# Kernel tuning notes

Hardware: AMD Instinct MI355X
Metric: run time of the kernel (lower is better)

The kernel has to match this reference:

```python
import math
import jax, jax.numpy as jnp
import numpy as np

NUM_HEADS = 32
HIDDEN = 4096
HEAD_DIM = HIDDEN // NUM_HEADS  # 128
NEG_INF = -1e30


def _alibi_slopes(n: int) -> jnp.ndarray:
    cp2 = 2 ** math.floor(math.log2(n))
    base = 2.0 ** (-(2.0 ** (-(math.log2(cp2) - 3))))
    slopes = base ** np.arange(1, cp2 + 1, dtype=np.float64)
    if cp2 != n:
        extra_base = 2.0 ** (-(2.0 ** (-(math.log2(2 * cp2) - 3))))
        rem = min(cp2, n - cp2)
        extra = extra_base ** np.arange(1, 1 + 2 * rem, 2, dtype=np.float64)
        slopes = np.concatenate([slopes, extra])
    return jnp.asarray(slopes, dtype=jnp.float32)


def setup_inputs() -> dict:
    key = jax.random.key(0)
    k1, k2, k3 = jax.random.split(key, 3)
    B, S = 2, 2048
    hidden_states = jax.random.normal(k1, (B, S, HIDDEN), dtype=jnp.float32)
    Wqkv = jax.random.normal(k2, (HIDDEN, NUM_HEADS * HEAD_DIM + 2 * HEAD_DIM), dtype=jnp.float32) * 0.02
    Wo = jax.random.normal(k3, (HIDDEN, HIDDEN), dtype=jnp.float32) * 0.02
    return {"hidden_states": hidden_states, "Wqkv": Wqkv, "Wo": Wo}


def reference(hidden_states, Wqkv, Wo):
    B, S, H = hidden_states.shape
    nH, d = NUM_HEADS, HEAD_DIM
    scale = d ** -0.5

    qkv = hidden_states @ Wqkv                      # [B,S,nH*d + 2d]
    q = qkv[..., : nH * d].reshape(B, S, nH, d)     # [B,S,nH,d]
    k = qkv[..., nH * d: nH * d + d]                # [B,S,d] (single kv head, MQA)
    v = qkv[..., nH * d + d:]                       # [B,S,d]

    scores = jnp.einsum("bqhd,bkd->bhqk", q, k) * scale  # [B,nH,S,S]

    pos_q = jnp.arange(S)[:, None]
    pos_k = jnp.arange(S)[None, :]
    slopes = _alibi_slopes(nH)                       # [nH]
    alibi = slopes[:, None, None] * (pos_k - pos_q).astype(jnp.float32)  # [nH,S,S]
    causal = pos_k <= pos_q                          # [S,S]

    scores = jnp.where(causal[None, None], scores + alibi[None], NEG_INF)
    probs = jax.nn.softmax(scores, axis=-1)
    attn = jnp.einsum("bhqk,bkd->bqhd", probs, v).reshape(B, S, H)
    return attn @ Wo
```

## Files before the change

kernel.cpp:

```cpp
#include <hip/hip_runtime.h>
#include <hip/hip_bf16.h>

typedef __attribute__((ext_vector_type(8))) short bf16x8;
typedef __attribute__((ext_vector_type(4))) float f32x4;
typedef __attribute__((ext_vector_type(8))) unsigned short u16x8;
typedef __attribute__((ext_vector_type(4))) unsigned short u16x4;

__device__ __forceinline__ unsigned short f2bf(float x) {
    union { float f; unsigned u; } v; v.f = x;
    unsigned r = v.u + 0x7fff + ((v.u >> 16) & 1);
    return (unsigned short)(r >> 16);
}

__device__ __forceinline__ unsigned short f2bf_hw(float x) {
    __hip_bfloat16 h = __float2bfloat16(x);
    return *reinterpret_cast<unsigned short*>(&h);
}

__device__ __forceinline__ void gload16(const void* g, void* l) {
    __builtin_amdgcn_global_load_lds(
        (const __attribute__((address_space(1))) void*)g,
        (__attribute__((address_space(3))) void*)l, 16, 0, 0);
}

__global__ __launch_bounds__(256) void cast_bf16_kernel(
    const float* __restrict__ src, unsigned short* __restrict__ dst, int n8) {
    int i = blockIdx.x * 256 + threadIdx.x;
    if (i >= n8) return;
    const float4* s = (const float4*)src + (size_t)i * 2;
    float4 a = s[0], b = s[1];
    u16x8 o;
    o[0] = f2bf(a.x); o[1] = f2bf(a.y); o[2] = f2bf(a.z); o[3] = f2bf(a.w);
    o[4] = f2bf(b.x); o[5] = f2bf(b.y); o[6] = f2bf(b.z); o[7] = f2bf(b.w);
    *(u16x8*)(dst + (size_t)i * 8) = o;
}

__global__ __launch_bounds__(256) void transpose_cast_kernel(
    const float* __restrict__ src, unsigned short* __restrict__ dst, int R, int C) {
    __shared__ float tile[32][33];
    const int bx = blockIdx.x * 32, by = blockIdx.y * 32;
    const int tx = threadIdx.x & 31, ty = threadIdx.x >> 5;
#pragma unroll
    for (int i = 0; i < 32; i += 8)
        tile[ty + i][tx] = src[(size_t)(by + ty + i) * C + (bx + tx)];
    __syncthreads();
#pragma unroll
    for (int i = 0; i < 32; i += 8)
        dst[(size_t)(bx + ty + i) * R + (by + tx)] = f2bf(tile[tx][ty + i]);
}

template <int OUTBF>
__global__ __launch_bounds__(256) void gemm_kernel(
    const unsigned short* __restrict__ A, const unsigned short* __restrict__ BT,
    void* __restrict__ Cp, int M, int N, int K) {
    __shared__ unsigned short Al[2][128 * 32];
    __shared__ unsigned short Bl[2][128 * 32];
    const int t = threadIdx.x;
    const int wid = t >> 6, lane = t & 63;
    const int l15 = lane & 15, lg = lane >> 4;
    const int bm = blockIdx.y * 128, bn = blockIdx.x * 128;
    const int wm = (wid >> 1) * 64, wn = (wid & 1) * 64;

    f32x4 acc[4][4];
#pragma unroll
    for (int i = 0; i < 4; ++i)
#pragma unroll
        for (int j = 0; j < 4; ++j) acc[i][j] = (f32x4)(0.f);

    const int nk = K >> 5;
    const int c0 = t, c1 = t + 256;

    auto stage = [&](int buf, int kt) {
        const unsigned short* Ab = A + (size_t)bm * K + kt * 32;
        const unsigned short* Bb = BT + (size_t)bn * K + kt * 32;
        gload16(Ab + (size_t)(c0 >> 2) * K + (c0 & 3) * 8, &Al[buf][wid * 64 * 8]);
        gload16(Ab + (size_t)(c1 >> 2) * K + (c1 & 3) * 8, &Al[buf][(256 + wid * 64) * 8]);
        gload16(Bb + (size_t)(c0 >> 2) * K + (c0 & 3) * 8, &Bl[buf][wid * 64 * 8]);
        gload16(Bb + (size_t)(c1 >> 2) * K + (c1 & 3) * 8, &Bl[buf][(256 + wid * 64) * 8]);
    };

    stage(0, 0);
    __syncthreads();
    for (int kt = 0; kt < nk; ++kt) {
        const int cur = kt & 1;
        if (kt + 1 < nk) stage(cur ^ 1, kt + 1);
        bf16x8 af[4], bfr[4];
#pragma unroll
        for (int i = 0; i < 4; ++i) {
            af[i]  = *(const bf16x8*)&Al[cur][(wm + i * 16 + l15) * 32 + lg * 8];
            bfr[i] = *(const bf16x8*)&Bl[cur][(wn + i * 16 + l15) * 32 + lg * 8];
        }
#pragma unroll
        for (int i = 0; i < 4; ++i)
#pragma unroll
            for (int j = 0; j < 4; ++j)
                acc[i][j] = __builtin_amdgcn_mfma_f32_16x16x32_bf16(af[i], bfr[j], acc[i][j], 0, 0, 0);
        __syncthreads();
    }

#pragma unroll
    for (int i = 0; i < 4; ++i)
#pragma unroll
        for (int j = 0; j < 4; ++j)
#pragma unroll
            for (int r = 0; r < 4; ++r) {
                const int row = bm + wm + i * 16 + lg * 4 + r;
                const int col = bn + wn + j * 16 + l15;
                if (OUTBF) ((unsigned short*)Cp)[(size_t)row * N + col] = f2bf(acc[i][j][r]);
                else       ((float*)Cp)[(size_t)row * N + col] = acc[i][j][r];
            }
}

__global__ __launch_bounds__(256, 4) void attn_kernel(
    const unsigned short* __restrict__ qkv, unsigned short* __restrict__ attn, int S) {
    constexpr int LD = 4352;
    __shared__ unsigned short Kl[64 * 128];
    __shared__ unsigned short Vt[128 * 64];
    __shared__ unsigned short Pl[4][16 * 64];
    const int t = threadIdx.x, wid = t >> 6;
    const int lane = t & 63, l15 = lane & 15, lg = lane >> 4;
    const int h = blockIdx.y, b = blockIdx.z;
    const size_t rb = (size_t)b * S;
    const int nQB = S >> 6;
    const float scale2 = 0.08838834764831845f * 1.4426950408889634f;
    const float slope2 = exp2f(-0.25f * (float)(h + 1)) * 1.4426950408889634f;
    const float sr1 = slope2, sr2 = slope2 * 2.f, sr3 = slope2 * 3.f;

    for (int half = 0; half < 2; ++half) {
        const int qblk = half ? (nQB - 1 - (int)blockIdx.x) : (int)blockIdx.x;
        const int q0w = qblk * 64 + wid * 16;
        const int qlane = q0w + l15;
        const float aq = slope2 * (float)qlane;

        bf16x8 qf[4];
        {
            const unsigned short* qrow = qkv + (rb + qlane) * LD + h * 128 + lg * 8;
#pragma unroll
            for (int j = 0; j < 4; ++j) qf[j] = *(const bf16x8*)(qrow + j * 32);
        }
        f32x4 o[8];
#pragma unroll
        for (int i = 0; i < 8; ++i) o[i] = (f32x4)(0.f);
        float m_ = -1e30f, l_ = 0.f;

        const int ntile = qblk + 1;
        for (int tile = 0; tile < ntile; ++tile) {
            const int t0 = tile * 64;
            {
                const char* kbase = (const char*)(qkv + (rb + t0) * LD + 4096);
#pragma unroll
                for (int i = 0; i < 4; ++i) {
                    const int c = i * 256 + t;
                    const int krow = c >> 4;
                    gload16(kbase + (size_t)krow * (LD * 2) + (((c & 15) * 16) ^ ((krow & 7) << 4)),
                            (char*)Kl + (i * 256 + wid * 64) * 16);
                }
            }
            {
                const unsigned short* vs = qkv + (rb + t0 + lane) * LD + 4224 + wid * 32;
                u16x8 v0 = *(const u16x8*)vs;
                u16x8 v1 = *(const u16x8*)(vs + 8);
                u16x8 v2 = *(const u16x8*)(vs + 16);
                u16x8 v3 = *(const u16x8*)(vs + 24);
                const int kb = 2 * lane;
#pragma unroll
                for (int e = 0; e < 8; ++e) {
                    int dd = wid * 32 + e;
                    *(unsigned short*)((char*)Vt + dd * 128 + (kb ^ ((dd & 7) << 4))) = v0[e];
                    dd += 8;
                    *(unsigned short*)((char*)Vt + dd * 128 + (kb ^ ((dd & 7) << 4))) = v1[e];
                    dd += 8;
                    *(unsigned short*)((char*)Vt + dd * 128 + (kb ^ ((dd & 7) << 4))) = v2[e];
                    dd += 8;
                    *(unsigned short*)((char*)Vt + dd * 128 + (kb ^ ((dd & 7) << 4))) = v3[e];
                }
            }
            __syncthreads();

            f32x4 s4[4];
#pragma unroll
            for (int ct = 0; ct < 4; ++ct) {
                s4[ct] = (f32x4)(0.f);
                const int row = ct * 16 + l15;
                const int swz = (row & 7) << 4;
#pragma unroll
                for (int j = 0; j < 4; ++j) {
                    bf16x8 kf = *(const bf16x8*)((const char*)Kl + row * 256 +
                                                 ((j * 64 + lg * 16) ^ swz));
                    s4[ct] = __builtin_amdgcn_mfma_f32_16x16x32_bf16(kf, qf[j], s4[ct], 0, 0, 0);
                }
            }

            const float base = slope2 * (float)(t0 + lg * 4) - aq;
            float p4[4][4];
            float mx = -1e30f;
            const bool lastt = (tile == ntile - 1);
            const int dbase = t0 + lg * 4 - qlane;
#pragma unroll
            for (int ct = 0; ct < 4; ++ct) {
                const float bbc = base + slope2 * 16.f * (float)ct;
#pragma unroll
                for (int r = 0; r < 4; ++r) {
                    float sc = fmaf(s4[ct][r], scale2,
                                    bbc + (r == 0 ? 0.f : (r == 1 ? sr1 : (r == 2 ? sr2 : sr3))));
                    if (lastt && (dbase + ct * 16 + r > 0)) sc = -1e30f;
                    p4[ct][r] = sc;
                    mx = fmaxf(mx, sc);
                }
            }
            mx = fmaxf(mx, __shfl_xor(mx, 16));
            mx = fmaxf(mx, __shfl_xor(mx, 32));

            if (!__all(mx <= m_ + 8.0f)) {
                const float mnew = fmaxf(m_, mx);
                const float corr = exp2f(m_ - mnew);
                m_ = mnew;
                l_ *= corr;
                float cr[4];
#pragma unroll
                for (int r = 0; r < 4; ++r) cr[r] = __shfl(corr, lg * 4 + r);
#pragma unroll
                for (int n = 0; n < 8; ++n) {
                    o[n][0] *= cr[0]; o[n][1] *= cr[1];
                    o[n][2] *= cr[2]; o[n][3] *= cr[3];
                }
            }

            float rs = 0.f;
#pragma unroll
            for (int ct = 0; ct < 4; ++ct)
#pragma unroll
                for (int r = 0; r < 4; ++r) {
                    const float pv = exp2f(p4[ct][r] - m_);
                    p4[ct][r] = pv;
                    rs += pv;
                }
            rs += __shfl_xor(rs, 16);
            rs += __shfl_xor(rs, 32);
            l_ += rs;

            {
                char* pb = (char*)&Pl[wid][0] + l15 * 128;
                const int swz = (l15 & 7) << 4;
#pragma unroll
                for (int ct = 0; ct < 4; ++ct) {
                    u16x4 w;
                    w[0] = f2bf_hw(p4[ct][0]); w[1] = f2bf_hw(p4[ct][1]);
                    w[2] = f2bf_hw(p4[ct][2]); w[3] = f2bf_hw(p4[ct][3]);
                    *(u16x4*)(pb + ((ct * 32 + lg * 8) ^ swz)) = w;
                }
            }

            const char* pb = (const char*)&Pl[wid][0] + l15 * 128;
            const int pswz = (l15 & 7) << 4;
            bf16x8 pa0 = *(const bf16x8*)(pb + ((lg * 16) ^ pswz));
            bf16x8 pa1 = *(const bf16x8*)(pb + ((64 + lg * 16) ^ pswz));
#pragma unroll
            for (int n = 0; n < 8; ++n) {
                const int dd = n * 16 + l15;
                const int vswz = (dd & 7) << 4;
                bf16x8 vf0 = *(const bf16x8*)((const char*)Vt + dd * 128 + ((lg * 16) ^ vswz));
                bf16x8 vf1 = *(const bf16x8*)((const char*)Vt + dd * 128 + ((64 + lg * 16) ^ vswz));
                f32x4 a4 = __builtin_amdgcn_mfma_f32_16x16x32_bf16(pa0, vf0, o[n], 0, 0, 0);
                o[n] = __builtin_amdgcn_mfma_f32_16x16x32_bf16(pa1, vf1, a4, 0, 0, 0);
            }
            __syncthreads();
        }

        const float rl = 1.f / l_;
        float rv[4];
#pragma unroll
        for (int r = 0; r < 4; ++r) rv[r] = __shfl(rl, lg * 4 + r);
#pragma unroll
        for (int n = 0; n < 8; ++n)
#pragma unroll
            for (int r = 0; r < 4; ++r) {
                const int q = q0w + lg * 4 + r;
                attn[(rb + q) * 4096 + h * 128 + n * 16 + l15] = f2bf(o[n][r] * rv[r]);
            }
    }
}

extern "C" void kernel_launch(void* const* d_in, const int* in_sizes, int n_in,
                              void* d_out, int out_size, void* d_ws, size_t ws_size,
                              hipStream_t stream) {
    const float* hidden = (const float*)d_in[0];
    const float* Wqkv   = (const float*)d_in[1];
    const float* Wo     = (const float*)d_in[2];
    float* out = (float*)d_out;
    char* ws = (char*)d_ws;

    const int B = 2, S = 2048, H = 4096, NQ = 4352;
    const int M = B * S;

    unsigned short* hb  = (unsigned short*)(ws);
    unsigned short* wT  = (unsigned short*)(ws + 33554432);
    unsigned short* qkv = (unsigned short*)(ws + 33554432 + 35651584);

    cast_bf16_kernel<<<(M * H / 8) / 256, 256, 0, stream>>>(hidden, hb, M * H / 8);
    transpose_cast_kernel<<<dim3(NQ / 32, H / 32), 256, 0, stream>>>(Wqkv, wT, H, NQ);
    gemm_kernel<1><<<dim3(NQ / 128, M / 128), 256, 0, stream>>>(hb, wT, qkv, M, NQ, H);
    transpose_cast_kernel<<<dim3(H / 32, H / 32), 256, 0, stream>>>(Wo, wT, H, H);
    attn_kernel<<<dim3(16, 32, 2), 256, 0, stream>>>(qkv, hb, S);
    gemm_kernel<0><<<dim3(H / 128, M / 128), 256, 0, stream>>>(hb, wT, out, M, H, H);
}
```

Baseline: 555.4 us.

## Add 256x256 pipelined GEMM kernel for output projection

Adds a new 512-thread GEMM kernel with 256x256 output tiles, double-buffered LDS staging via direct global-to-LDS loads, and swizzled LDS layout. It interleaves staging of the next K-tile with MFMA sub-blocks under fine-grained barriers and priority hints, plus an XCD-aware block-to-tile mapping. It replaces the 128x128 GEMM for the Wo projection to raise data reuse and hide load latency. It risks register pressure from the large accumulator set and assumes fixed dimensions (4096x4096, grid hard-coded to 256 blocks).

After: 554.9 us. No clear change (-0.1%).

```diff
diff --git a/kernel.cpp b/kernel.cpp
--- a/kernel.cpp
+++ b/kernel.cpp
@@ -108,6 +108,137 @@
                 const int col = bn + wn + j * 16 + l15;
                 if (OUTBF) ((unsigned short*)Cp)[(size_t)row * N + col] = f2bf(acc[i][j][r]);
                 else       ((float*)Cp)[(size_t)row * N + col] = acc[i][j][r];
+            }
+}
+
+#define SYNC1() do { __builtin_amdgcn_s_barrier(); \
+    asm volatile("s_waitcnt lgkmcnt(0)" ::: "memory"); } while (0)
+#define GATE6() do { asm volatile("s_waitcnt vmcnt(6)" ::: "memory"); \
+    __builtin_amdgcn_s_barrier(); __builtin_amdgcn_sched_barrier(0); } while (0)
+
+template <int OUTBF>
+__global__ __launch_bounds__(512, 2) void gemm256_kernel(
+    const unsigned short* __restrict__ A, const unsigned short* __restrict__ BT,
+    void* __restrict__ Cp, int K, int N) {
+    __shared__ __align__(16) char lds[131072];
+    const int t = threadIdx.x;
+    const int wid = t >> 6, lane = t & 63;
+    const int l15 = lane & 15, lg = lane >> 4;
+    const int xcd = blockIdx.x & 7, idx = blockIdx.x >> 3;
+    const int bm = ((xcd >> 1) * 4 + (idx >> 3)) * 256;
+    const int bn = ((xcd & 1) * 8 + (idx & 7)) * 256;
+    const int wmh = wid >> 2;
+    const int wq  = wid & 3;
+    const int bhf = wq >> 1;
+    const int br0 = (wq & 1) * 64;
+
+    auto Ab = [&](int b, int h) -> char* { return lds + ((b * 2 + h) << 14); };
+    auto Bb = [&](int b, int h) -> char* { return lds + 65536 + ((b * 2 + h) << 14); };
+
+    auto stage = [&](char* halfBase, const unsigned short* mat, int rowBase, int kt) {
+#pragma unroll
+        for (int j = 0; j < 2; ++j) {
+            const int dbase = ((j << 3) + wid) << 10;
+            const int q = (dbase + lane * 16) ^ (lane & 32);
+            const int p = q >> 13, r = (q >> 6) & 127, cb = q & 63;
+            gload16(mat + (size_t)(rowBase + r) * K + (kt << 6) + (p << 5) + (cb >> 1),
+                    halfBase + dbase);
+        }
+    };
+
+    f32x4 acc[8][4];
+#pragma unroll
+    for (int i = 0; i < 8; ++i)
+#pragma unroll
+        for (int j = 0; j < 4; ++j) acc[i][j] = (f32x4)(0.f);
+
+    bf16x8 af[8][2];
+    bf16x8 bfr[2][2];
+
+    auto ldA = [&](int b) {
+        const char* base = Ab(b, wmh);
+#pragma unroll
+        for (int i = 0; i < 8; ++i) {
+            const int r = i * 16 + l15;
+            const int sw = ((r >> 3) & 1) << 5;
+#pragma unroll
+            for (int kk = 0; kk < 2; ++kk)
+                af[i][kk] = *(const bf16x8*)(base + ((kk * 8192 + r * 64 + lg * 16) ^ sw));
+        }
+    };
+    auto ldB = [&](int b, int nh) {
+        const char* base = Bb(b, bhf);
+#pragma unroll
+        for (int i = 0; i < 2; ++i) {
+            const int r = br0 + (nh * 2 + i) * 16 + l15;
+            const int sw = ((r >> 3) & 1) << 5;
+#pragma unroll
+            for (int kk = 0; kk < 2; ++kk)
+                bfr[i][kk] = *(const bf16x8*)(base + ((kk * 8192 + r * 64 + lg * 16) ^ sw));
+        }
+    };
+    auto MF = [&](int mh, int nh) {
+        __builtin_amdgcn_s_setprio(1);
+#pragma unroll
+        for (int i = 0; i < 4; ++i)
+#pragma unroll
+            for (int j = 0; j < 2; ++j)
+#pragma unroll
+                for (int kk = 0; kk < 2; ++kk)
+                    acc[mh * 4 + i][nh * 2 + j] = __builtin_amdgcn_mfma_f32_16x16x32_bf16(
+                        af[mh * 4 + i][kk], bfr[j][kk], acc[mh * 4 + i][nh * 2 + j], 0, 0, 0);
+        __builtin_amdgcn_s_setprio(0);
+    };
+
+    stage(Ab(0, 0), A, bm, 0);
+    stage(Ab(0, 1), A, bm + 128, 0);
+    stage(Bb(0, 0), BT, bn, 0);
+    stage(Bb(0, 1), BT, bn + 128, 0);
+    stage(Ab(1, 0), A, bm, 1);
+    stage(Ab(1, 1), A, bm + 128, 1);
+    stage(Bb(1, 0), BT, bn, 1);
+    asm volatile("s_waitcnt vmcnt(6)" ::: "memory");
+    __builtin_amdgcn_s_barrier();
+    __builtin_amdgcn_sched_barrier(0);
+
+    const int kmask = (K >> 6) - 1;
+    const int niter = K >> 7;
+    for (int it = 0; it < niter; ++it) {
+        const int kto = 2 * it + 1;
+        const int kne = (2 * it + 2) & kmask;
+        const int kno = (2 * it + 3) & kmask;
+        ldA(0); ldB(0, 0);
+        stage(Bb(1, 1), BT, bn + 128, kto);
+        SYNC1(); MF(0, 0); __builtin_amdgcn_s_barrier();
+        stage(Ab(0, 0), A, bm, kne);
+        SYNC1(); MF(1, 0); __builtin_amdgcn_s_barrier();
+        ldB(0, 1);
+        stage(Ab(0, 1), A, bm + 128, kne);
+        SYNC1(); MF(1, 1); __builtin_amdgcn_s_barrier();
+        stage(Bb(0, 0), BT, bn, kne);
+        SYNC1(); MF(0, 1); GATE6();
+        ldA(1); ldB(1, 0);
+        stage(Bb(0, 1), BT, bn + 128, kne);
+        SYNC1(); MF(0, 0); __builtin_amdgcn_s_barrier();
+        stage(Ab(1, 0), A, bm, kno);
+        SYNC1(); MF(1, 0); __builtin_amdgcn_s_barrier();
+        ldB(1, 1);
+        stage(Ab(1, 1), A, bm + 128, kno);
+        SYNC1(); MF(1, 1); __builtin_amdgcn_s_barrier();
+        stage(Bb(1, 0), BT, bn, kno);
+        SYNC1(); MF(0, 1); GATE6();
+    }
+
+#pragma unroll
+    for (int mi = 0; mi < 8; ++mi)
+#pragma unroll
+        for (int ni = 0; ni < 4; ++ni)
+#pragma unroll
+            for (int rr = 0; rr < 4; ++rr) {
+                const size_t off = (size_t)(bm + wmh * 128 + mi * 16 + lg * 4 + rr) * N +
+                                   bn + wq * 64 + ni * 16 + l15;
+                if (OUTBF) ((unsigned short*)Cp)[off] = f2bf(acc[mi][ni][rr]);
+                else       ((float*)Cp)[off] = acc[mi][ni][rr];
             }
 }
 
@@ -302,5 +433,5 @@
     gemm_kernel<1><<<dim3(NQ / 128, M / 128), 256, 0, stream>>>(hb, wT, qkv, M, NQ, H);
     transpose_cast_kernel<<<dim3(H / 32, H / 32), 256, 0, stream>>>(Wo, wT, H, H);
     attn_kernel<<<dim3(16, 32, 2), 256, 0, stream>>>(qkv, hb, S);
-    gemm_kernel<0><<<dim3(H / 128, M / 128), 256, 0, stream>>>(hb, wT, out, M, H, H);
-}
+    gemm256_kernel<0><<<dim3(256), 512, 0, stream>>>(hb, wT, out, H, H);
+}
```
